# Kernel optimization log

Hardware: AMD Instinct MI355X
Metric: run time of the kernel (lower is better)

## Reference

```python
import jax, jax.numpy as jnp
import numpy as np

N_NODES = 100000
N_FEATURES = 512
N_HIDDEN = 256
N_EDGES = 3200000


def setup_inputs() -> dict:
    key = jax.random.key(0)
    k_x, k_r, k_c, k_v, k_w, k_b = jax.random.split(key, 6)
    x = jax.random.normal(k_x, (1, N_NODES, N_FEATURES), dtype=jnp.float32)
    adj_rows = jax.random.randint(k_r, (N_EDGES,), 0, N_NODES, dtype=jnp.int32)
    adj_cols = jax.random.randint(k_c, (N_EDGES,), 0, N_NODES, dtype=jnp.int32)
    adj_vals = jax.random.uniform(k_v, (N_EDGES,), dtype=jnp.float32)
    # Linear params: xavier_normal_ on weight [H, F], default bias init
    std = float(np.sqrt(2.0 / (N_FEATURES + N_HIDDEN)))
    W = jax.random.normal(k_w, (N_HIDDEN, N_FEATURES), dtype=jnp.float32) * std
    bound = float(1.0 / np.sqrt(N_FEATURES))
    b = jax.random.uniform(k_b, (N_HIDDEN,), dtype=jnp.float32, minval=-bound, maxval=bound)
    alpha = jnp.asarray(0.25, dtype=jnp.float32)  # PReLU default single-param init
    return {"x": x, "adj_rows": adj_rows, "adj_cols": adj_cols,
            "adj_vals": adj_vals, "W": W, "b": b, "alpha": alpha}


def reference(x, adj_rows, adj_cols, adj_vals, W, b, alpha):
    # Linear: [1, N, F] @ [F, H] + [H] -> squeeze to [N, H]
    h = (jnp.einsum('bnf,hf->bnh', x, W) + b)[0]
    # spmm(adj, h): gather source rows, scale by edge value, scatter-add to dest rows
    msgs = adj_vals[:, None] * h[adj_cols]              # [E, H]
    agg = jax.ops.segment_sum(msgs, adj_rows, num_segments=N_NODES)  # [N, H]
    out = jnp.where(agg >= 0, agg, alpha * agg)         # PReLU
    return out[None]                                     # [1, N, H]
```

## Files before the change

### kernel.cpp

```cpp
#include <hip/hip_runtime.h>


#define K_DIM 512
#define H_DIM 256

#define BIN_ROWS 512
#define NBIN_MAX 256
#define EB 18432
#define P1_CHUNK 4096
#define P1_PER_T 4
#define SPU 8

typedef __attribute__((ext_vector_type(8))) short short8;
typedef __attribute__((ext_vector_type(4))) float floatx4;

__device__ inline short f32_to_bf16(float f) {
    unsigned u = __float_as_uint(f);
    u += 0x7fffu + ((u >> 16) & 1u);
    return (short)(u >> 16);
}
__device__ inline float bf16_to_f32(unsigned short u) {
    return __uint_as_float(((unsigned)u) << 16);
}

__global__ __launch_bounds__(256) void convert_w_kernel(
    const float* __restrict__ W, unsigned short* __restrict__ Wbf)
{
    int i = (blockIdx.x * 256 + threadIdx.x) * 8;
    float4 a = *(const float4*)(W + i);
    float4 b = *(const float4*)(W + i + 4);
    short8 v;
    v[0] = f32_to_bf16(a.x); v[1] = f32_to_bf16(a.y);
    v[2] = f32_to_bf16(a.z); v[3] = f32_to_bf16(a.w);
    v[4] = f32_to_bf16(b.x); v[5] = f32_to_bf16(b.y);
    v[6] = f32_to_bf16(b.z); v[7] = f32_to_bf16(b.w);
    *(short8*)((short*)Wbf + i) = v;
}

#define GT_M 128
#define GT_K 32
#define NSTEP (K_DIM / GT_K)
#define LDSW 32

__global__ __launch_bounds__(512, 4) void gemm_bf16_kernel(
    const float* __restrict__ A,
    const unsigned short* __restrict__ Wbf,
    const float* __restrict__ bias,
    unsigned short* __restrict__ H,
    int M)
{
    __shared__ short As[GT_M * LDSW];

    const int tid  = threadIdx.x;
    const int m0   = blockIdx.x * GT_M;

    const int wave = tid >> 6;
    const int lane = tid & 63;
    const int wm   = (wave >> 2) * 64;
    const int wn   = (wave & 3) * 64;
    const int quad = lane >> 4;
    const int l16  = lane & 15;

    const int arow  = tid >> 2;
    const int apart = tid & 3;

    floatx4 acc[4][4] = {};

    const bool arow_ok = (m0 + arow) < M;
    const float* asrc = A + (size_t)(m0 + arow) * K_DIM + apart * 8;

    float f[8];
    if (arow_ok) {
        *(float4*)(f + 0) = *(const float4*)(asrc + 0);
        *(float4*)(f + 4) = *(const float4*)(asrc + 4);
    } else {
        #pragma unroll
        for (int j = 0; j < 8; ++j) f[j] = 0.f;
    }

    for (int ks = 0; ks < NSTEP; ++ks) {
        short8 v;
        #pragma unroll
        for (int j = 0; j < 8; ++j) v[j] = f32_to_bf16(f[j]);
        *(short8*)&As[arow * LDSW + apart * 8] = v;
        __syncthreads();

        if (ks + 1 < NSTEP && arow_ok) {
            const float* s2 = asrc + (ks + 1) * GT_K;
            *(float4*)(f + 0) = *(const float4*)(s2 + 0);
            *(float4*)(f + 4) = *(const float4*)(s2 + 4);
        }

        short8 bf[4];
        const int kb = ks * GT_K + quad * 8;
        #pragma unroll
        for (int t = 0; t < 4; ++t)
            bf[t] = *(const short8*)(Wbf + (size_t)(wn + t * 16 + l16) * K_DIM + kb);

        short8 af[4];
        #pragma unroll
        for (int t = 0; t < 4; ++t)
            af[t] = *(const short8*)&As[(wm + t * 16 + l16) * LDSW + quad * 8];

        #pragma unroll
        for (int i = 0; i < 4; ++i)
            #pragma unroll
            for (int j = 0; j < 4; ++j)
                acc[i][j] = __builtin_amdgcn_mfma_f32_16x16x32_bf16(af[i], bf[j], acc[i][j], 0, 0, 0);
        __syncthreads();
    }

    #pragma unroll
    for (int j = 0; j < 4; ++j) {
        int gcol = wn + j * 16 + l16;
        float bj = bias[gcol];
        #pragma unroll
        for (int i = 0; i < 4; ++i) {
            int rbase = m0 + wm + i * 16 + quad * 4;
            #pragma unroll
            for (int r = 0; r < 4; ++r) {
                int gm = rbase + r;
                if (gm < M)
                    H[(size_t)gm * H_DIM + gcol] =
                        (unsigned short)f32_to_bf16(acc[i][j][r] + bj);
            }
        }
    }
}

__global__ __launch_bounds__(1024) void partition_kernel(
    const int* __restrict__ rows, const int* __restrict__ cols,
    const float* __restrict__ vals, int* __restrict__ binCursor,
    int2* __restrict__ binned, int E, int nbins)
{
    __shared__ int hist[NBIN_MAX];
    __shared__ int binOff[NBIN_MAX];
    __shared__ int gbase[NBIN_MAX];
    __shared__ int cursor[NBIN_MAX];
    __shared__ int sc[2][NBIN_MAX];
    __shared__ int2 stage[P1_CHUNK];
    __shared__ unsigned char binOf[P1_CHUNK];

    const int tid = threadIdx.x;
    const int e0  = blockIdx.x * P1_CHUNK;
    const int total = min(P1_CHUNK, E - e0);

    int r[P1_PER_T], c[P1_PER_T];
    float v[P1_PER_T];
    #pragma unroll
    for (int i = 0; i < P1_PER_T; ++i) {
        int e = e0 + tid + i * 1024;
        if (e < E) { r[i] = rows[e]; c[i] = cols[e]; v[i] = vals[e]; }
        else       { r[i] = -1; c[i] = 0; v[i] = 0.f; }
    }

    if (tid < NBIN_MAX) hist[tid] = 0;
    __syncthreads();
    #pragma unroll
    for (int i = 0; i < P1_PER_T; ++i)
        if (r[i] >= 0) atomicAdd(&hist[r[i] >> 9], 1);
    __syncthreads();

    if (tid < NBIN_MAX) sc[0][tid] = hist[tid];
    __syncthreads();
    int cur = 0;
    for (int d = 1; d < NBIN_MAX; d <<= 1) {
        if (tid < NBIN_MAX) {
            int y = sc[cur][tid];
            if (tid >= d) y += sc[cur][tid - d];
            sc[cur ^ 1][tid] = y;
        }
        __syncthreads();
        cur ^= 1;
    }
    if (tid < NBIN_MAX) {
        int x    = hist[tid];
        int excl = sc[cur][tid] - x;
        binOff[tid] = excl;
        cursor[tid] = excl;
        if (tid < nbins) gbase[tid] = atomicAdd(&binCursor[tid], x);
        else             gbase[tid] = 0;
    }
    __syncthreads();

    #pragma unroll
    for (int i = 0; i < P1_PER_T; ++i) {
        if (r[i] >= 0) {
            int bin  = r[i] >> 9;
            int lpos = atomicAdd(&cursor[bin], 1);
            stage[lpos] = make_int2(((r[i] & (BIN_ROWS - 1)) << 17) | c[i],
                                    __float_as_int(v[i]));
            binOf[lpos] = (unsigned char)bin;
        }
    }
    __syncthreads();

    #pragma unroll
    for (int i = 0; i < P1_PER_T; ++i) {
        int idx = tid + i * 1024;
        if (idx < total) {
            int bin = binOf[idx];
            int rel = gbase[bin] + (idx - binOff[bin]);
            if (rel < EB)
                binned[(size_t)bin * EB + rel] = stage[idx];
        }
    }
}

__global__ __launch_bounds__(1024) void binsort_kernel(
    const int2* __restrict__ binned, const int* __restrict__ binCursor,
    int2* __restrict__ sorted, int* __restrict__ rowstart,
    int* __restrict__ degArr, int M)
{
    __shared__ int hist[BIN_ROWS];
    __shared__ int cursor[BIN_ROWS];
    __shared__ int sc[2][BIN_ROWS];

    const int b   = blockIdx.x;
    const int tid = threadIdx.x;
    int cnt = binCursor[b]; if (cnt > EB) cnt = EB;
    int rows_here = M - b * BIN_ROWS; if (rows_here > BIN_ROWS) rows_here = BIN_ROWS;

    if (tid < BIN_ROWS) hist[tid] = 0;
    __syncthreads();
    const int2* src = binned + (size_t)b * EB;
    for (int i = tid; i < cnt; i += 1024)
        atomicAdd(&hist[((unsigned)src[i].x) >> 17], 1);
    __syncthreads();

    if (tid < BIN_ROWS) sc[0][tid] = hist[tid];
    __syncthreads();
    int cur = 0;
    for (int d = 1; d < BIN_ROWS; d <<= 1) {
        if (tid < BIN_ROWS) {
            int y = sc[cur][tid];
            if (tid >= d) y += sc[cur][tid - d];
            sc[cur ^ 1][tid] = y;
        }
        __syncthreads();
        cur ^= 1;
    }
    if (tid < BIN_ROWS) {
        int x    = hist[tid];
        int excl = sc[cur][tid] - x;
        cursor[tid] = excl;
        if (tid < rows_here) {
            rowstart[b * BIN_ROWS + tid] = b * EB + excl;
            degArr[b * BIN_ROWS + tid]   = x;
        }
    }
    __syncthreads();

    int2* dst = sorted + (size_t)b * EB;
    for (int i = tid; i < cnt; i += 1024) {
        int2 p  = src[i];
        int rl  = ((unsigned)p.x) >> 17;
        int pos = atomicAdd(&cursor[rl], 1);
        dst[pos] = make_int2(p.x & 0x1FFFF, p.y);
    }
}

__global__ __launch_bounds__(256) void spmm_gather_kernel(
    const unsigned short* __restrict__ h, const int* __restrict__ rowstart,
    const int* __restrict__ degArr, const int2* __restrict__ sorted,
    const float* __restrict__ alpha_p, float* __restrict__ out, int M)
{
    const int wave = threadIdx.x >> 6;
    const int lane = threadIdx.x & 63;
    const int row = blockIdx.x * 4 + wave;
    if (row >= M) return;

    const int deg = degArr[row];
    const int2* ep = sorted + rowstart[row];

    float4 acc = make_float4(0.f, 0.f, 0.f, 0.f);

    for (int chunk = 0; chunk < deg; chunk += 64) {
        int rem = deg - chunk;
        int n   = rem < 64 ? rem : 64;
        int ru  = (n + SPU - 1) & ~(SPU - 1);
        int2 p  = (chunk + lane < deg) ? ep[chunk + lane] : make_int2(0, 0);

        ushort4 u[SPU]; float vv[SPU];
        #pragma unroll
        for (int j = 0; j < SPU; ++j) {
            int c  = __shfl(p.x, j);
            vv[j]  = __int_as_float(__shfl(p.y, j));
            u[j]   = *(const ushort4*)(h + (size_t)c * H_DIM + lane * 4);
        }
        for (int e = SPU; e < ru; e += SPU) {
            ushort4 u2[SPU]; float vv2[SPU];
            #pragma unroll
            for (int j = 0; j < SPU; ++j) {
                int c   = __shfl(p.x, e + j);
                vv2[j]  = __int_as_float(__shfl(p.y, e + j));
                u2[j]   = *(const ushort4*)(h + (size_t)c * H_DIM + lane * 4);
            }
            #pragma unroll
            for (int j = 0; j < SPU; ++j) {
                float v = vv[j];
                acc.x += v * bf16_to_f32(u[j].x);
                acc.y += v * bf16_to_f32(u[j].y);
                acc.z += v * bf16_to_f32(u[j].z);
                acc.w += v * bf16_to_f32(u[j].w);
            }
            #pragma unroll
            for (int j = 0; j < SPU; ++j) { u[j] = u2[j]; vv[j] = vv2[j]; }
        }
        #pragma unroll
        for (int j = 0; j < SPU; ++j) {
            float v = vv[j];
            acc.x += v * bf16_to_f32(u[j].x);
            acc.y += v * bf16_to_f32(u[j].y);
            acc.z += v * bf16_to_f32(u[j].z);
            acc.w += v * bf16_to_f32(u[j].w);
        }
    }

    const float alpha = *alpha_p;
    acc.x = acc.x >= 0.f ? acc.x : alpha * acc.x;
    acc.y = acc.y >= 0.f ? acc.y : alpha * acc.y;
    acc.z = acc.z >= 0.f ? acc.z : alpha * acc.z;
    acc.w = acc.w >= 0.f ? acc.w : alpha * acc.w;
    *(float4*)(out + (size_t)row * H_DIM + lane * 4) = acc;
}

extern "C" void kernel_launch(void* const* d_in, const int* in_sizes, int n_in,
                              void* d_out, int out_size, void* d_ws, size_t ws_size,
                              hipStream_t stream) {
    const float* x        = (const float*)d_in[0];
    const int*   adj_rows = (const int*)d_in[1];
    const int*   adj_cols = (const int*)d_in[2];
    const float* adj_vals = (const float*)d_in[3];
    const float* W        = (const float*)d_in[4];
    const float* b        = (const float*)d_in[5];
    const float* alpha    = (const float*)d_in[6];
    float* out = (float*)d_out;

    const int M = in_sizes[0] / K_DIM;
    const int E = in_sizes[1];
    const int nbins = (M + BIN_ROWS - 1) / BIN_ROWS;

    char* ws = (char*)d_ws;
    size_t off = 0;
    auto alloc = [&](size_t bytes) {
        char* p = ws + off;
        off += (bytes + 255) & ~(size_t)255;
        return p;
    };
    unsigned short* h = (unsigned short*)alloc((size_t)M * H_DIM * sizeof(unsigned short));
    int2* binned  = (int2*)alloc((size_t)nbins * EB * sizeof(int2));
    int2* sorted  = (int2*)alloc((size_t)nbins * EB * sizeof(int2));
    int*  rowstart = (int*)alloc((size_t)M * sizeof(int));
    int*  degArr   = (int*)alloc((size_t)M * sizeof(int));
    int*  binCursor = (int*)alloc((size_t)NBIN_MAX * sizeof(int));
    unsigned short* Wbf = (unsigned short*)alloc((size_t)H_DIM * K_DIM * sizeof(unsigned short));

    convert_w_kernel<<<64, 256, 0, stream>>>(W, Wbf);

    gemm_bf16_kernel<<<dim3((M + GT_M - 1) / GT_M, 1), 512, 0, stream>>>(x, Wbf, b, h, M);

    hipMemsetAsync(binCursor, 0, (size_t)NBIN_MAX * sizeof(int), stream);
    partition_kernel<<<(E + P1_CHUNK - 1) / P1_CHUNK, 1024, 0, stream>>>(
        adj_rows, adj_cols, adj_vals, binCursor, binned, E, nbins);

    binsort_kernel<<<nbins, 1024, 0, stream>>>(binned, binCursor, sorted,
                                               rowstart, degArr, M);

    spmm_gather_kernel<<<(M + 3) / 4, 256, 0, stream>>>(h, rowstart, degArr, sorted,
                                                        alpha, out, M);
}
```

Measured before the change: 664.3 us.

## Fuse bin sort into SpMM via LDS per half-bin; stage W tiles in LDS

Merges the binsort and gather kernels into one kernel. Each block takes half of a 512-row bin, counting-sorts that half's edges into shared memory and then gathers bf16 h rows per destination row. This drops the global sorted array and the rowstart/degree buffers along with their round trip, but it needs about 72KB of LDS per block, reads each bin twice, and silently truncates any half-bin holding more than 9216 edges. The GEMM now stages the bf16 W tile in LDS instead of loading it straight from global memory per wave, and the partition kernel uses 512 threads with 8 edges per thread.

```diff
diff --git a/kernel.cpp b/kernel.cpp
--- a/kernel.cpp
+++ b/kernel.cpp
@@ -8,8 +8,9 @@
 #define NBIN_MAX 256
 #define EB 18432
 #define P1_CHUNK 4096
-#define P1_PER_T 4
-#define SPU 8
+#define P1_PER_T 8
+#define HALF_ROWS 256
+#define SCAP 9216
 
 typedef __attribute__((ext_vector_type(8))) short short8;
 typedef __attribute__((ext_vector_type(4))) float floatx4;
@@ -50,6 +51,7 @@
     int M)
 {
     __shared__ short As[GT_M * LDSW];
+    __shared__ short Bs[256 * LDSW];
 
     const int tid  = threadIdx.x;
     const int m0   = blockIdx.x * GT_M;
@@ -61,15 +63,17 @@
     const int quad = lane >> 4;
     const int l16  = lane & 15;
 
-    const int arow  = tid >> 2;
-    const int apart = tid & 3;
+    const int arow = tid >> 2;
+    const int seg  = tid & 3;
 
     floatx4 acc[4][4] = {};
 
     const bool arow_ok = (m0 + arow) < M;
-    const float* asrc = A + (size_t)(m0 + arow) * K_DIM + apart * 8;
+    const float* asrc = A + (size_t)(m0 + arow) * K_DIM + seg * 8;
+    const unsigned short* bsrc = Wbf + (size_t)arow * K_DIM + seg * 8;
 
     float f[8];
+    short8 g0, g1;
     if (arow_ok) {
         *(float4*)(f + 0) = *(const float4*)(asrc + 0);
         *(float4*)(f + 4) = *(const float4*)(asrc + 4);
@@ -77,31 +81,36 @@
         #pragma unroll
         for (int j = 0; j < 8; ++j) f[j] = 0.f;
     }
+    g0 = *(const short8*)(bsrc);
+    g1 = *(const short8*)(bsrc + 128 * K_DIM);
 
     for (int ks = 0; ks < NSTEP; ++ks) {
         short8 v;
         #pragma unroll
         for (int j = 0; j < 8; ++j) v[j] = f32_to_bf16(f[j]);
-        *(short8*)&As[arow * LDSW + apart * 8] = v;
+        *(short8*)&As[arow * LDSW + seg * 8] = v;
+        *(short8*)&Bs[arow * LDSW + seg * 8] = g0;
+        *(short8*)&Bs[(arow + 128) * LDSW + seg * 8] = g1;
         __syncthreads();
 
-        if (ks + 1 < NSTEP && arow_ok) {
-            const float* s2 = asrc + (ks + 1) * GT_K;
-            *(float4*)(f + 0) = *(const float4*)(s2 + 0);
-            *(float4*)(f + 4) = *(const float4*)(s2 + 4);
-        }
-
-        short8 bf[4];
-        const int kb = ks * GT_K + quad * 8;
-        #pragma unroll
-        for (int t = 0; t < 4; ++t)
-            bf[t] = *(const short8*)(Wbf + (size_t)(wn + t * 16 + l16) * K_DIM + kb);
-
-        short8 af[4];
+        if (ks + 1 < NSTEP) {
+            if (arow_ok) {
+                const float* s2 = asrc + (ks + 1) * GT_K;
+                *(float4*)(f + 0) = *(const float4*)(s2 + 0);
+                *(float4*)(f + 4) = *(const float4*)(s2 + 4);
+            }
+            const unsigned short* b2 = bsrc + (ks + 1) * GT_K;
+            g0 = *(const short8*)(b2);
+            g1 = *(const short8*)(b2 + 128 * K_DIM);
+        }
+
+        short8 af[4], bf[4];
         #pragma unroll
         for (int t = 0; t < 4; ++t)
             af[t] = *(const short8*)&As[(wm + t * 16 + l16) * LDSW + quad * 8];
-
+        #pragma unroll
+        for (int t = 0; t < 4; ++t)
+            bf[t] = *(const short8*)&Bs[(wn + t * 16 + l16) * LDSW + quad * 8];
         #pragma unroll
         for (int i = 0; i < 4; ++i)
             #pragma unroll
@@ -128,7 +137,7 @@
     }
 }
 
-__global__ __launch_bounds__(1024) void partition_kernel(
+__global__ __launch_bounds__(512) void partition_kernel(
     const int* __restrict__ rows, const int* __restrict__ cols,
     const float* __restrict__ vals, int* __restrict__ binCursor,
     int2* __restrict__ binned, int E, int nbins)
@@ -149,7 +158,7 @@
     float v[P1_PER_T];
     #pragma unroll
     for (int i = 0; i < P1_PER_T; ++i) {
-        int e = e0 + tid + i * 1024;
+        int e = e0 + tid + i * 512;
         if (e < E) { r[i] = rows[e]; c[i] = cols[e]; v[i] = vals[e]; }
         else       { r[i] = -1; c[i] = 0; v[i] = 0.f; }
     }
@@ -197,7 +206,7 @@
 
     #pragma unroll
     for (int i = 0; i < P1_PER_T; ++i) {
-        int idx = tid + i * 1024;
+        int idx = tid + i * 512;
         if (idx < total) {
             int bin = binOf[idx];
             int rel = gbase[bin] + (idx - binOff[bin]);
@@ -207,32 +216,37 @@
     }
 }
 
-__global__ __launch_bounds__(1024) void binsort_kernel(
+__global__ __launch_bounds__(512, 2) void spmm_bin_kernel(
     const int2* __restrict__ binned, const int* __restrict__ binCursor,
-    int2* __restrict__ sorted, int* __restrict__ rowstart,
-    int* __restrict__ degArr, int M)
+    const unsigned short* __restrict__ h, const float* __restrict__ alpha_p,
+    float* __restrict__ out, int M)
 {
-    __shared__ int hist[BIN_ROWS];
-    __shared__ int cursor[BIN_ROWS];
-    __shared__ int sc[2][BIN_ROWS];
-
-    const int b   = blockIdx.x;
-    const int tid = threadIdx.x;
+    __shared__ int2 run[SCAP];
+    __shared__ int hist[HALF_ROWS];
+    __shared__ int rstart[HALF_ROWS];
+    __shared__ int cursor[HALF_ROWS];
+    __shared__ int sc[2][HALF_ROWS];
+
+    const int b    = blockIdx.x >> 1;
+    const int half = blockIdx.x & 1;
+    const int tid  = threadIdx.x;
     int cnt = binCursor[b]; if (cnt > EB) cnt = EB;
-    int rows_here = M - b * BIN_ROWS; if (rows_here > BIN_ROWS) rows_here = BIN_ROWS;
-
-    if (tid < BIN_ROWS) hist[tid] = 0;
-    __syncthreads();
+
+    if (tid < HALF_ROWS) hist[tid] = 0;
+    __syncthreads();
+
     const int2* src = binned + (size_t)b * EB;
-    for (int i = tid; i < cnt; i += 1024)
-        atomicAdd(&hist[((unsigned)src[i].x) >> 17], 1);
-    __syncthreads();
-
-    if (tid < BIN_ROWS) sc[0][tid] = hist[tid];
+    for (int i = tid; i < cnt; i += 512) {
+        int rl = ((unsigned)src[i].x) >> 17;
+        if ((rl >> 8) == half) atomicAdd(&hist[rl & 255], 1);
+    }
+    __syncthreads();
+
+    if (tid < HALF_ROWS) sc[0][tid] = hist[tid];
     __syncthreads();
     int cur = 0;
-    for (int d = 1; d < BIN_ROWS; d <<= 1) {
-        if (tid < BIN_ROWS) {
+    for (int d = 1; d < HALF_ROWS; d <<= 1) {
+        if (tid < HALF_ROWS) {
             int y = sc[cur][tid];
             if (tid >= d) y += sc[cur][tid - d];
             sc[cur ^ 1][tid] = y;
@@ -240,89 +254,74 @@
         __syncthreads();
         cur ^= 1;
     }
-    if (tid < BIN_ROWS) {
-        int x    = hist[tid];
-        int excl = sc[cur][tid] - x;
+    if (tid < HALF_ROWS) {
+        int excl = sc[cur][tid] - hist[tid];
+        rstart[tid] = excl;
         cursor[tid] = excl;
-        if (tid < rows_here) {
-            rowstart[b * BIN_ROWS + tid] = b * EB + excl;
-            degArr[b * BIN_ROWS + tid]   = x;
-        }
-    }
-    __syncthreads();
-
-    int2* dst = sorted + (size_t)b * EB;
-    for (int i = tid; i < cnt; i += 1024) {
-        int2 p  = src[i];
-        int rl  = ((unsigned)p.x) >> 17;
-        int pos = atomicAdd(&cursor[rl], 1);
-        dst[pos] = make_int2(p.x & 0x1FFFF, p.y);
-    }
-}
-
-__global__ __launch_bounds__(256) void spmm_gather_kernel(
-    const unsigned short* __restrict__ h, const int* __restrict__ rowstart,
-    const int* __restrict__ degArr, const int2* __restrict__ sorted,
-    const float* __restrict__ alpha_p, float* __restrict__ out, int M)
-{
-    const int wave = threadIdx.x >> 6;
-    const int lane = threadIdx.x & 63;
-    const int row = blockIdx.x * 4 + wave;
-    if (row >= M) return;
-
-    const int deg = degArr[row];
-    const int2* ep = sorted + rowstart[row];
-
-    float4 acc = make_float4(0.f, 0.f, 0.f, 0.f);
-
-    for (int chunk = 0; chunk < deg; chunk += 64) {
-        int rem = deg - chunk;
-        int n   = rem < 64 ? rem : 64;
-        int ru  = (n + SPU - 1) & ~(SPU - 1);
-        int2 p  = (chunk + lane < deg) ? ep[chunk + lane] : make_int2(0, 0);
-
-        ushort4 u[SPU]; float vv[SPU];
-        #pragma unroll
-        for (int j = 0; j < SPU; ++j) {
-            int c  = __shfl(p.x, j);
-            vv[j]  = __int_as_float(__shfl(p.y, j));
-            u[j]   = *(const ushort4*)(h + (size_t)c * H_DIM + lane * 4);
-        }
-        for (int e = SPU; e < ru; e += SPU) {
-            ushort4 u2[SPU]; float vv2[SPU];
-            #pragma unroll
-            for (int j = 0; j < SPU; ++j) {
-                int c   = __shfl(p.x, e + j);
-                vv2[j]  = __int_as_float(__shfl(p.y, e + j));
-                u2[j]   = *(const ushort4*)(h + (size_t)c * H_DIM + lane * 4);
+    }
+    __syncthreads();
+
+    for (int i = tid; i < cnt; i += 512) {
+        int2 p = src[i];
+        int rl = ((unsigned)p.x) >> 17;
+        if ((rl >> 8) == half) {
+            int pos = atomicAdd(&cursor[rl & 255], 1);
+            if (pos < SCAP) run[pos] = make_int2(p.x & 0x1FFFF, p.y);
+        }
+    }
+    __syncthreads();
+
+    const int wave = tid >> 6;
+    const int lane = tid & 63;
+    const float alpha = *alpha_p;
+    const int growbase = b * BIN_ROWS + half * HALF_ROWS;
+
+    for (int rr = wave; rr < HALF_ROWS; rr += 8) {
+        int grow = growbase + rr;
+        if (grow >= M) break;
+        int st  = rstart[rr];
+        int den = st + hist[rr];
+        if (den > SCAP) den = SCAP;
+        int deg = den - st;
+
+        float4 acc = make_float4(0.f, 0.f, 0.f, 0.f);
+        int e = 0;
+        for (; e + 8 <= deg; e += 8) {
+            int cc[8]; float vv[8];
+            #pragma unroll
+            for (int j = 0; j < 8; ++j) {
+                int2 p = run[st + e + j];
+                cc[j] = p.x; vv[j] = __int_as_float(p.y);
             }
-            #pragma unroll
-            for (int j = 0; j < SPU; ++j) {
+            ushort4 u[8];
+            #pragma unroll
+            for (int j = 0; j < 8; ++j)
+                u[j] = *(const ushort4*)(h + (size_t)cc[j] * H_DIM + lane * 4);
+            #pragma unroll
+            for (int j = 0; j < 8; ++j) {
                 float v = vv[j];
                 acc.x += v * bf16_to_f32(u[j].x);
                 acc.y += v * bf16_to_f32(u[j].y);
                 acc.z += v * bf16_to_f32(u[j].z);
                 acc.w += v * bf16_to_f32(u[j].w);
             }
-            #pragma unroll
-            for (int j = 0; j < SPU; ++j) { u[j] = u2[j]; vv[j] = vv2[j]; }
-        }
-        #pragma unroll
-        for (int j = 0; j < SPU; ++j) {
-            float v = vv[j];
-            acc.x += v * bf16_to_f32(u[j].x);
-            acc.y += v * bf16_to_f32(u[j].y);
-            acc.z += v * bf16_to_f32(u[j].z);
-            acc.w += v * bf16_to_f32(u[j].w);
-        }
-    }
-
-    const float alpha = *alpha_p;
-    acc.x = acc.x >= 0.f ? acc.x : alpha * acc.x;
-    acc.y = acc.y >= 0.f ? acc.y : alpha * acc.y;
-    acc.z = acc.z >= 0.f ? acc.z : alpha * acc.z;
-    acc.w = acc.w >= 0.f ? acc.w : alpha * acc.w;
-    *(float4*)(out + (size_t)row * H_DIM + lane * 4) = acc;
+        }
+        for (; e < deg; ++e) {
+            int2 p = run[st + e];
+            float v = __int_as_float(p.y);
+            ushort4 u = *(const ushort4*)(h + (size_t)p.x * H_DIM + lane * 4);
+            acc.x += v * bf16_to_f32(u.x);
+            acc.y += v * bf16_to_f32(u.y);
+            acc.z += v * bf16_to_f32(u.z);
+            acc.w += v * bf16_to_f32(u.w);
+        }
+
+        acc.x = acc.x >= 0.f ? acc.x : alpha * acc.x;
+        acc.y = acc.y >= 0.f ? acc.y : alpha * acc.y;
+        acc.z = acc.z >= 0.f ? acc.z : alpha * acc.z;
+        acc.w = acc.w >= 0.f ? acc.w : alpha * acc.w;
+        *(float4*)(out + (size_t)grow * H_DIM + lane * 4) = acc;
+    }
 }
 
 extern "C" void kernel_launch(void* const* d_in, const int* in_sizes, int n_in,
@@ -350,9 +349,6 @@
     };
     unsigned short* h = (unsigned short*)alloc((size_t)M * H_DIM * sizeof(unsigned short));
     int2* binned  = (int2*)alloc((size_t)nbins * EB * sizeof(int2));
-    int2* sorted  = (int2*)alloc((size_t)nbins * EB * sizeof(int2));
-    int*  rowstart = (int*)alloc((size_t)M * sizeof(int));
-    int*  degArr   = (int*)alloc((size_t)M * sizeof(int));
     int*  binCursor = (int*)alloc((size_t)NBIN_MAX * sizeof(int));
     unsigned short* Wbf = (unsigned short*)alloc((size_t)H_DIM * K_DIM * sizeof(unsigned short));
 
@@ -361,12 +357,8 @@
     gemm_bf16_kernel<<<dim3((M + GT_M - 1) / GT_M, 1), 512, 0, stream>>>(x, Wbf, b, h, M);
 
     hipMemsetAsync(binCursor, 0, (size_t)NBIN_MAX * sizeof(int), stream);
-    partition_kernel<<<(E + P1_CHUNK - 1) / P1_CHUNK, 1024, 0, stream>>>(
+    partition_kernel<<<(E + P1_CHUNK - 1) / P1_CHUNK, 512, 0, stream>>>(
         adj_rows, adj_cols, adj_vals, binCursor, binned, E, nbins);
 
-    binsort_kernel<<<nbins, 1024, 0, stream>>>(binned, binCursor, sorted,
-                                               rowstart, degArr, M);
-
-    spmm_gather_kernel<<<(M + 3) / 4, 256, 0, stream>>>(h, rowstart, degArr, sorted,
-                                                        alpha, out, M);
-}
+    spmm_bin_kernel<<<nbins * 2, 512, 0, stream>>>(binned, binCursor, h, alpha, out, M);
+}
```

Result: faster. 643.5 us (-3.1%).
